# Kernel tuning notes

Hardware: AMD Instinct MI355X
Metric: run time of the kernel (lower is better)

Reference implementation:

```python
import jax, jax.numpy as jnp
import numpy as np

N = 65536          # nodes
E = N * 7          # edges (avg_degree = n_edge_type = 7)
C_IN = 128
C_OUT = 128
N_EDGE_TYPE = 7
N_NODE_TYPE = 5
FEAT = C_IN + N_NODE_TYPE  # 133, channels after one-hot concat


def setup_inputs() -> dict:
    key = jax.random.key(0)
    k1, k2, k3, k4, k5 = jax.random.split(key, 5)
    x = jax.random.normal(k1, (N, C_IN), dtype=jnp.float32)
    edge_idx = jax.random.randint(k2, (2, E), 0, N, dtype=jnp.int64)
    edge_type = jax.random.randint(k3, (E,), 0, N_EDGE_TYPE, dtype=jnp.int64)
    node_type = jax.random.randint(k4, (N,), 0, N_NODE_TYPE, dtype=jnp.int64)
    # uniform init a la module's reset_parameters
    fan_in = 7 * C_IN
    fan_out = 7 * C_OUT
    a = np.sqrt(3.0) * np.sqrt(2.0 / (fan_in + fan_out))
    weights = jax.random.uniform(k5, (N_EDGE_TYPE * FEAT, C_OUT), dtype=jnp.float32,
                                 minval=-a, maxval=a)
    return {"x": x, "edge_idx": edge_idx, "edge_type": edge_type,
            "node_type": node_type, "weights": weights}


def reference(x, edge_idx, edge_type, node_type, weights):
    # one-hot node type concat (n_node_type > 1 branch)
    one_hot = jax.nn.one_hot(node_type, N_NODE_TYPE, dtype=x.dtype)
    xa = jnp.concatenate([x, one_hot], axis=1)          # [N, FEAT]
    row, col = edge_idx[0], edge_idx[1]
    seg = row * N_EDGE_TYPE + edge_type                 # [E]
    gathered = xa[col]                                  # [E, FEAT]
    num_seg = N * N_EDGE_TYPE
    sums = jax.ops.segment_sum(gathered, seg, num_segments=num_seg)
    cnt = jax.ops.segment_sum(jnp.ones((E,), dtype=xa.dtype), seg, num_segments=num_seg)
    col_data = sums / jnp.maximum(cnt, 1.0)[:, None]    # scatter_mean
    # overwrite self-loop slot (last edge type) with node's own features
    self_idx = jnp.arange(N, dtype=jnp.int64) * N_EDGE_TYPE + (N_EDGE_TYPE - 1)
    col_data = col_data.at[self_idx].set(xa)
    out = col_data.reshape(N, N_EDGE_TYPE * FEAT) @ weights  # [N, C_OUT]
    return out
```

## Files before the change

### kernel.cpp

```cpp
#include <hip/hip_runtime.h>
#include <hip/hip_bf16.h>

#define N_NODES 65536
#define N_EDGES (N_NODES * 7)
#define NSEG    (N_NODES * 7)
#define CAP     12
#define ZROW    65536

typedef short short8 __attribute__((ext_vector_type(8)));
typedef float f32x4  __attribute__((ext_vector_type(4)));

__device__ __forceinline__ unsigned short f2bf(float f) {
    return __builtin_bit_cast(unsigned short, (__bf16)f);
}
__device__ __forceinline__ unsigned pack2(float lo, float hi) {
    return (unsigned)f2bf(lo) | ((unsigned)f2bf(hi) << 16);
}
__device__ __forceinline__ float bflo(unsigned d) { return __uint_as_float(d << 16); }
__device__ __forceinline__ float bfhi(unsigned d) { return __uint_as_float(d & 0xffff0000u); }

__global__ __launch_bounds__(256) void k_big(const float* __restrict__ x,
                                             const int* __restrict__ eidx,
                                             const int* __restrict__ etype,
                                             const int* __restrict__ ntype,
                                             const float* __restrict__ W,
                                             unsigned short* __restrict__ xb,
                                             unsigned short* __restrict__ wb,
                                             unsigned* __restrict__ seg32,
                                             unsigned short* __restrict__ scol) {
    int i = blockIdx.x * 256 + threadIdx.x;

    if (i < N_EDGES) {
        int t = etype[i];
        if (t < 6) {
            int r = eidx[i];
            int c = eidx[N_EDGES + i];
            int u = ntype[c];
            unsigned seg = (unsigned)r * 7u + (unsigned)t;
            unsigned inc = 1u | (1u << (7 + 5 * u));
            unsigned old = atomicAdd(&seg32[seg], inc);
            unsigned slot = old & 0x7fu;
            if (slot < CAP) scol[seg * CAP + slot] = (unsigned short)c;
        }
    }

    {
        int row = i >> 4, mm = i & 15;
        const f32x4* p = reinterpret_cast<const f32x4*>(x + (size_t)row * 128 + mm * 8);
        f32x4 v0 = p[0], v1 = p[1];
        uint4 w;
        w.x = pack2(v0[0], v0[1]); w.y = pack2(v0[2], v0[3]);
        w.z = pack2(v1[0], v1[1]); w.w = pack2(v1[2], v1[3]);
        reinterpret_cast<uint4*>(xb)[i] = w;
    }

    if (i < 16) reinterpret_cast<uint4*>(xb + (size_t)ZROW * 128)[i] = (uint4){0u, 0u, 0u, 0u};

    if (i < 143360) {
        int j    = i & 7;
        int lane = (i >> 3) & 63;
        int cb   = (i >> 9) & 7;
        int tkc  = i >> 12;
        int kc   = tkc % 5;
        int t    = tkc / 5;
        int k = kc * 32 + ((lane >> 4) << 3) + j;
        int c = cb * 16 + (lane & 15);
        float v = (k < 133) ? W[(t * 133 + k) * 128 + c] : 0.0f;
        wb[i] = f2bf(v);
    }
}

__global__ __launch_bounds__(512, 4) void k_main(const unsigned short* __restrict__ xb,
                                                 const int* __restrict__ ntype,
                                                 const unsigned* __restrict__ seg32,
                                                 const unsigned short* __restrict__ scol,
                                                 const unsigned short* __restrict__ wb,
                                                 float* __restrict__ out) {
    __shared__ unsigned short sA[3 * 64 * 168];

    const int tid  = threadIdx.x;
    const int lane = tid & 63;
    const int wid  = tid >> 6;
    const int n0   = blockIdx.x * 64;
    const int r    = tid >> 3;
    const int m    = tid & 7;
    const int n    = n0 + r;
    const int wswz = ((r >> 3) & 1) << 5;

    if (tid < 192) {
        uint4 z = {0u, 0u, 0u, 0u};
        *reinterpret_cast<uint4*>(sA + tid * 168 + 136) = z;
        *reinterpret_cast<uint4*>(sA + tid * 168 + 144) = z;
        *reinterpret_cast<uint4*>(sA + tid * 168 + 152) = z;
    }

    unsigned sv[6], c_t[6];
    uint2 q2[6];
    #pragma unroll
    for (int t = 0; t < 6; ++t) {
        sv[t]  = seg32[n * 7 + t];
        c_t[t] = sv[t] & 0x7fu;
        q2[t]  = *reinterpret_cast<const uint2*>(scol + ((size_t)n * 7 + t) * CAP);
    }
    const int ntS = ntype[n];

    auto addrow = [&](float* f, unsigned col) {
        const short8* p = reinterpret_cast<const short8*>(xb + (size_t)col * 128 + m * 16);
        short8 v0 = p[0], v1 = p[1];
        uint4 u0 = *reinterpret_cast<const uint4*>(&v0);
        uint4 u1 = *reinterpret_cast<const uint4*>(&v1);
        f[0] += bflo(u0.x); f[1] += bfhi(u0.x); f[2]  += bflo(u0.y); f[3]  += bfhi(u0.y);
        f[4] += bflo(u0.z); f[5] += bfhi(u0.z); f[6]  += bflo(u0.w); f[7]  += bfhi(u0.w);
        f[8] += bflo(u1.x); f[9] += bfhi(u1.x); f[10] += bflo(u1.y); f[11] += bfhi(u1.y);
        f[12]+= bflo(u1.z); f[13]+= bfhi(u1.z); f[14] += bflo(u1.w); f[15] += bfhi(u1.w);
    };

    auto build_tile = [&](int t, int tile) {
        const unsigned cntv = c_t[t];
        const float inv = (cntv > 1u) ? __builtin_amdgcn_rcpf((float)cntv) : 1.0f;
        unsigned cA = (cntv >= 1u) ? (q2[t].x & 0xffffu) : (unsigned)ZROW;
        unsigned cB = (cntv >= 2u) ? (q2[t].x >> 16)     : (unsigned)ZROW;
        const short8* pA = reinterpret_cast<const short8*>(xb + (size_t)cA * 128 + m * 16);
        const short8* pB = reinterpret_cast<const short8*>(xb + (size_t)cB * 128 + m * 16);
        short8 a0 = pA[0], a1 = pA[1];
        short8 b0 = pB[0], b1 = pB[1];
        uint4 w0, w1;
        if (cntv <= 1u) {
            w0 = *reinterpret_cast<const uint4*>(&a0);
            w1 = *reinterpret_cast<const uint4*>(&a1);
        } else {
            uint4 ua0 = *reinterpret_cast<const uint4*>(&a0);
            uint4 ua1 = *reinterpret_cast<const uint4*>(&a1);
            uint4 ub0 = *reinterpret_cast<const uint4*>(&b0);
            uint4 ub1 = *reinterpret_cast<const uint4*>(&b1);
            float f[16];
            f[0] = bflo(ua0.x)+bflo(ub0.x); f[1] = bfhi(ua0.x)+bfhi(ub0.x);
            f[2] = bflo(ua0.y)+bflo(ub0.y); f[3] = bfhi(ua0.y)+bfhi(ub0.y);
            f[4] = bflo(ua0.z)+bflo(ub0.z); f[5] = bfhi(ua0.z)+bfhi(ub0.z);
            f[6] = bflo(ua0.w)+bflo(ub0.w); f[7] = bfhi(ua0.w)+bfhi(ub0.w);
            f[8] = bflo(ua1.x)+bflo(ub1.x); f[9] = bfhi(ua1.x)+bfhi(ub1.x);
            f[10]= bflo(ua1.y)+bflo(ub1.y); f[11]= bfhi(ua1.y)+bfhi(ub1.y);
            f[12]= bflo(ua1.z)+bflo(ub1.z); f[13]= bfhi(ua1.z)+bfhi(ub1.z);
            f[14]= bflo(ua1.w)+bflo(ub1.w); f[15]= bfhi(ua1.w)+bfhi(ub1.w);
            if (cntv >= 3u) {
                const unsigned ce = (cntv < (unsigned)CAP) ? cntv : (unsigned)CAP;
                addrow(f, q2[t].y & 0xffffu);
                if (ce >= 4u) {
                    addrow(f, q2[t].y >> 16);
                    const size_t segbase = ((size_t)n * 7 + t) * CAP;
                    for (unsigned e = 4; e < ce; ++e)
                        addrow(f, (unsigned)scol[segbase + e]);
                }
            }
            w0.x = pack2(f[0]*inv,  f[1]*inv);  w0.y = pack2(f[2]*inv,  f[3]*inv);
            w0.z = pack2(f[4]*inv,  f[5]*inv);  w0.w = pack2(f[6]*inv,  f[7]*inv);
            w1.x = pack2(f[8]*inv,  f[9]*inv);  w1.y = pack2(f[10]*inv, f[11]*inv);
            w1.z = pack2(f[12]*inv, f[13]*inv); w1.w = pack2(f[14]*inv, f[15]*inv);
        }
        const int base = (tile * 64 + r) * 168;
        const int o = (m * 16) ^ wswz;
        *reinterpret_cast<uint4*>(sA + base + o)     = w0;
        *reinterpret_cast<uint4*>(sA + base + o + 8) = w1;
        if (m == 0) {
            float g0 = (float)((sv[t] >> 7)  & 31u) * inv;
            float g1 = (float)((sv[t] >> 12) & 31u) * inv;
            float g2 = (float)((sv[t] >> 17) & 31u) * inv;
            float g3 = (float)((sv[t] >> 22) & 31u) * inv;
            float g4 = (float)((sv[t] >> 27) & 31u) * inv;
            uint4 wo;
            wo.x = pack2(g0, g1); wo.y = pack2(g2, g3);
            wo.z = pack2(g4, 0.f); wo.w = 0u;
            *reinterpret_cast<uint4*>(sA + base + 128) = wo;
        }
    };

    auto build_self = [&](int tile) {
        const short8* p = reinterpret_cast<const short8*>(xb + (size_t)n * 128 + m * 16);
        short8 s0 = p[0], s1 = p[1];
        const int base = (tile * 64 + r) * 168;
        const int o = (m * 16) ^ wswz;
        *reinterpret_cast<uint4*>(sA + base + o)     = *reinterpret_cast<const uint4*>(&s0);
        *reinterpret_cast<uint4*>(sA + base + o + 8) = *reinterpret_cast<const uint4*>(&s1);
        if (m == 0) {
            uint4 wo;
            wo.x = pack2((float)(ntS == 0), (float)(ntS == 1));
            wo.y = pack2((float)(ntS == 2), (float)(ntS == 3));
            wo.z = pack2((float)(ntS == 4), 0.f);
            wo.w = 0u;
            *reinterpret_cast<uint4*>(sA + base + 128) = wo;
        }
    };

    const int arl  = lane & 15;
    const int g8   = (lane >> 4) << 3;
    const int rswz = ((lane >> 3) & 1) << 5;
    f32x4 acc[4];
    #pragma unroll
    for (int st = 0; st < 4; ++st) acc[st] = (f32x4){0.f, 0.f, 0.f, 0.f};

    auto marathon = [&](int slot, int bt) {
        short8 bv[5];
        #pragma unroll
        for (int kc = 0; kc < 5; ++kc)
            bv[kc] = *reinterpret_cast<const short8*>(
                wb + ((((bt * 5 + kc) * 8 + wid) << 6) + lane) * 8);
        #pragma unroll
        for (int kc = 0; kc < 5; ++kc) {
            const int off = (kc < 4) ? ((kc * 32 + g8) ^ rswz) : (128 + g8);
            #pragma unroll
            for (int st = 0; st < 4; ++st) {
                short8 av = *reinterpret_cast<const short8*>(
                    sA + (slot * 64 + st * 16 + arl) * 168 + off);
                acc[st] = __builtin_amdgcn_mfma_f32_16x16x32_bf16(av, bv[kc], acc[st], 0, 0, 0);
            }
        }
    };

    build_tile(0, 0);
    build_tile(1, 1);
    build_self(2);
    __syncthreads();
    marathon(0, 0); marathon(1, 1); marathon(2, 6);
    __syncthreads();

    build_tile(2, 0);
    build_tile(3, 1);
    __syncthreads();
    marathon(0, 2); marathon(1, 3);
    __syncthreads();

    build_tile(4, 0);
    build_tile(5, 1);
    __syncthreads();
    marathon(0, 4); marathon(1, 5);

    const int ocol = (wid << 4) + (lane & 15);
    const int ro   = ((lane >> 4) << 2);
    #pragma unroll
    for (int st = 0; st < 4; ++st) {
        #pragma unroll
        for (int rr = 0; rr < 4; ++rr) {
            out[(size_t)(n0 + st * 16 + ro + rr) * 128 + ocol] = acc[st][rr];
        }
    }
}


extern "C" void kernel_launch(void* const* d_in, const int* in_sizes, int n_in,
                              void* d_out, int out_size, void* d_ws, size_t ws_size,
                              hipStream_t stream) {
    const float* x     = (const float*)d_in[0];
    const int*   eidx  = (const int*)d_in[1];
    const int*   etype = (const int*)d_in[2];
    const int*   ntype = (const int*)d_in[3];
    const float* W     = (const float*)d_in[4];
    float* out = (float*)d_out;

    unsigned short* xb    = (unsigned short*)d_ws;
    unsigned short* wb    = (unsigned short*)((char*)d_ws + 16777472);
    unsigned*       seg32 = (unsigned*)((char*)d_ws + 17064192);
    unsigned short* scol  = (unsigned short*)((char*)d_ws + 18899200);

    hipMemsetAsync(seg32, 0, NSEG * sizeof(unsigned), stream);
    k_big <<<4096,         256, 0, stream>>>(x, eidx, etype, ntype, W, xb, wb, seg32, scol);
    k_main<<<N_NODES / 64, 512, 0, stream>>>(xb, ntype, seg32, scol, wb, out);
}
```

Before: 83.53 us.

## Split main kernel into producer/consumer waves with double-buffered LDS tiles

Reworks k_main so that four waves gather and average neighbour rows into a double-buffered shared tile while the other four waves run MFMAs on the previous edge-type tile. The block now covers 32 nodes instead of 64, LDS shrinks, and launch bounds rise to 6 blocks per CU. The aim is to overlap the irregular gather latency with matrix compute and raise occupancy. In exchange only half the waves do MFMA, there are more barriers per block, weights are reloaded per 32 rows, and the LDS XOR swizzle was removed, which may add bank conflicts.

```diff
diff --git a/kernel.cpp b/kernel.cpp
--- a/kernel.cpp
+++ b/kernel.cpp
@@ -70,80 +70,73 @@
     }
 }
 
-__global__ __launch_bounds__(512, 4) void k_main(const unsigned short* __restrict__ xb,
+__global__ __launch_bounds__(512, 6) void k_main(const unsigned short* __restrict__ xb,
                                                  const int* __restrict__ ntype,
                                                  const unsigned* __restrict__ seg32,
                                                  const unsigned short* __restrict__ scol,
                                                  const unsigned short* __restrict__ wb,
                                                  float* __restrict__ out) {
-    __shared__ unsigned short sA[3 * 64 * 168];
+    __shared__ unsigned short sA[2][32][168];
 
     const int tid  = threadIdx.x;
     const int lane = tid & 63;
     const int wid  = tid >> 6;
-    const int n0   = blockIdx.x * 64;
-    const int r    = tid >> 3;
-    const int m    = tid & 7;
-    const int n    = n0 + r;
-    const int wswz = ((r >> 3) & 1) << 5;
+    const int n0   = blockIdx.x * 32;
+    const bool consumer = (wid >= 4);
 
     if (tid < 192) {
-        uint4 z = {0u, 0u, 0u, 0u};
-        *reinterpret_cast<uint4*>(sA + tid * 168 + 136) = z;
-        *reinterpret_cast<uint4*>(sA + tid * 168 + 144) = z;
-        *reinterpret_cast<uint4*>(sA + tid * 168 + 152) = z;
-    }
-
-    unsigned sv[6], c_t[6];
-    uint2 q2[6];
-    #pragma unroll
-    for (int t = 0; t < 6; ++t) {
-        sv[t]  = seg32[n * 7 + t];
-        c_t[t] = sv[t] & 0x7fu;
-        q2[t]  = *reinterpret_cast<const uint2*>(scol + ((size_t)n * 7 + t) * CAP);
-    }
-    const int ntS = ntype[n];
+        int j = tid % 3, sr = tid / 3;
+        *reinterpret_cast<uint4*>(&sA[sr >> 5][sr & 31][136 + j * 8]) =
+            (uint4){0u, 0u, 0u, 0u};
+    }
+
+    const int r = (tid >> 3) & 31;
+    const int m = tid & 7;
+    const int n = n0 + r;
+    unsigned sv[6]; uint2 q2[6]; int ntS = 0;
+    if (!consumer) {
+        #pragma unroll
+        for (int t = 0; t < 6; ++t) {
+            sv[t] = seg32[n * 7 + t];
+            q2[t] = *reinterpret_cast<const uint2*>(scol + ((size_t)n * 7 + t) * CAP);
+        }
+        ntS = ntype[n];
+    }
 
     auto addrow = [&](float* f, unsigned col) {
-        const short8* p = reinterpret_cast<const short8*>(xb + (size_t)col * 128 + m * 16);
-        short8 v0 = p[0], v1 = p[1];
-        uint4 u0 = *reinterpret_cast<const uint4*>(&v0);
-        uint4 u1 = *reinterpret_cast<const uint4*>(&v1);
+        const uint4* p = reinterpret_cast<const uint4*>(xb + (size_t)col * 128 + m * 16);
+        uint4 u0 = p[0], u1 = p[1];
         f[0] += bflo(u0.x); f[1] += bfhi(u0.x); f[2]  += bflo(u0.y); f[3]  += bfhi(u0.y);
         f[4] += bflo(u0.z); f[5] += bfhi(u0.z); f[6]  += bflo(u0.w); f[7]  += bfhi(u0.w);
         f[8] += bflo(u1.x); f[9] += bfhi(u1.x); f[10] += bflo(u1.y); f[11] += bfhi(u1.y);
         f[12]+= bflo(u1.z); f[13]+= bfhi(u1.z); f[14] += bflo(u1.w); f[15] += bfhi(u1.w);
     };
 
-    auto build_tile = [&](int t, int tile) {
-        const unsigned cntv = c_t[t];
-        const float inv = (cntv > 1u) ? __builtin_amdgcn_rcpf((float)cntv) : 1.0f;
-        unsigned cA = (cntv >= 1u) ? (q2[t].x & 0xffffu) : (unsigned)ZROW;
-        unsigned cB = (cntv >= 2u) ? (q2[t].x >> 16)     : (unsigned)ZROW;
-        const short8* pA = reinterpret_cast<const short8*>(xb + (size_t)cA * 128 + m * 16);
-        const short8* pB = reinterpret_cast<const short8*>(xb + (size_t)cB * 128 + m * 16);
-        short8 a0 = pA[0], a1 = pA[1];
-        short8 b0 = pB[0], b1 = pB[1];
+    auto build_tile = [&](int t, int slot) {
+        const unsigned svt = sv[t];
+        const unsigned cnt = svt & 0x7fu;
+        const float inv = (cnt > 1u) ? __builtin_amdgcn_rcpf((float)cnt) : 1.0f;
+        unsigned c0 = (cnt >= 1u) ? (q2[t].x & 0xffffu) : (unsigned)ZROW;
+        unsigned c1 = (cnt >= 2u) ? (q2[t].x >> 16)     : (unsigned)ZROW;
+        const uint4* p0 = reinterpret_cast<const uint4*>(xb + (size_t)c0 * 128 + m * 16);
+        const uint4* p1 = reinterpret_cast<const uint4*>(xb + (size_t)c1 * 128 + m * 16);
+        uint4 a0 = p0[0], a1 = p0[1];
+        uint4 b0 = p1[0], b1 = p1[1];
         uint4 w0, w1;
-        if (cntv <= 1u) {
-            w0 = *reinterpret_cast<const uint4*>(&a0);
-            w1 = *reinterpret_cast<const uint4*>(&a1);
+        if (cnt <= 1u) {
+            w0 = a0; w1 = a1;
         } else {
-            uint4 ua0 = *reinterpret_cast<const uint4*>(&a0);
-            uint4 ua1 = *reinterpret_cast<const uint4*>(&a1);
-            uint4 ub0 = *reinterpret_cast<const uint4*>(&b0);
-            uint4 ub1 = *reinterpret_cast<const uint4*>(&b1);
             float f[16];
-            f[0] = bflo(ua0.x)+bflo(ub0.x); f[1] = bfhi(ua0.x)+bfhi(ub0.x);
-            f[2] = bflo(ua0.y)+bflo(ub0.y); f[3] = bfhi(ua0.y)+bfhi(ub0.y);
-            f[4] = bflo(ua0.z)+bflo(ub0.z); f[5] = bfhi(ua0.z)+bfhi(ub0.z);
-            f[6] = bflo(ua0.w)+bflo(ub0.w); f[7] = bfhi(ua0.w)+bfhi(ub0.w);
-            f[8] = bflo(ua1.x)+bflo(ub1.x); f[9] = bfhi(ua1.x)+bfhi(ub1.x);
-            f[10]= bflo(ua1.y)+bflo(ub1.y); f[11]= bfhi(ua1.y)+bfhi(ub1.y);
-            f[12]= bflo(ua1.z)+bflo(ub1.z); f[13]= bfhi(ua1.z)+bfhi(ub1.z);
-            f[14]= bflo(ua1.w)+bflo(ub1.w); f[15]= bfhi(ua1.w)+bfhi(ub1.w);
-            if (cntv >= 3u) {
-                const unsigned ce = (cntv < (unsigned)CAP) ? cntv : (unsigned)CAP;
+            f[0] = bflo(a0.x)+bflo(b0.x); f[1] = bfhi(a0.x)+bfhi(b0.x);
+            f[2] = bflo(a0.y)+bflo(b0.y); f[3] = bfhi(a0.y)+bfhi(b0.y);
+            f[4] = bflo(a0.z)+bflo(b0.z); f[5] = bfhi(a0.z)+bfhi(b0.z);
+            f[6] = bflo(a0.w)+bflo(b0.w); f[7] = bfhi(a0.w)+bfhi(b0.w);
+            f[8] = bflo(a1.x)+bflo(b1.x); f[9] = bfhi(a1.x)+bfhi(b1.x);
+            f[10]= bflo(a1.y)+bflo(b1.y); f[11]= bfhi(a1.y)+bfhi(b1.y);
+            f[12]= bflo(a1.z)+bflo(b1.z); f[13]= bfhi(a1.z)+bfhi(b1.z);
+            f[14]= bflo(a1.w)+bflo(b1.w); f[15]= bfhi(a1.w)+bfhi(b1.w);
+            if (cnt >= 3u) {
+                const unsigned ce = (cnt < (unsigned)CAP) ? cnt : (unsigned)CAP;
                 addrow(f, q2[t].y & 0xffffu);
                 if (ce >= 4u) {
                     addrow(f, q2[t].y >> 16);
@@ -157,90 +150,82 @@
             w1.x = pack2(f[8]*inv,  f[9]*inv);  w1.y = pack2(f[10]*inv, f[11]*inv);
             w1.z = pack2(f[12]*inv, f[13]*inv); w1.w = pack2(f[14]*inv, f[15]*inv);
         }
-        const int base = (tile * 64 + r) * 168;
-        const int o = (m * 16) ^ wswz;
-        *reinterpret_cast<uint4*>(sA + base + o)     = w0;
-        *reinterpret_cast<uint4*>(sA + base + o + 8) = w1;
+        uint4* dst = reinterpret_cast<uint4*>(&sA[slot][r][m * 16]);
+        dst[0] = w0;
+        dst[1] = w1;
         if (m == 0) {
-            float g0 = (float)((sv[t] >> 7)  & 31u) * inv;
-            float g1 = (float)((sv[t] >> 12) & 31u) * inv;
-            float g2 = (float)((sv[t] >> 17) & 31u) * inv;
-            float g3 = (float)((sv[t] >> 22) & 31u) * inv;
-            float g4 = (float)((sv[t] >> 27) & 31u) * inv;
+            float g0 = (float)((svt >> 7)  & 31u) * inv;
+            float g1 = (float)((svt >> 12) & 31u) * inv;
+            float g2 = (float)((svt >> 17) & 31u) * inv;
+            float g3 = (float)((svt >> 22) & 31u) * inv;
+            float g4 = (float)((svt >> 27) & 31u) * inv;
             uint4 wo;
             wo.x = pack2(g0, g1); wo.y = pack2(g2, g3);
             wo.z = pack2(g4, 0.f); wo.w = 0u;
-            *reinterpret_cast<uint4*>(sA + base + 128) = wo;
+            *reinterpret_cast<uint4*>(&sA[slot][r][128]) = wo;
         }
     };
 
-    auto build_self = [&](int tile) {
-        const short8* p = reinterpret_cast<const short8*>(xb + (size_t)n * 128 + m * 16);
-        short8 s0 = p[0], s1 = p[1];
-        const int base = (tile * 64 + r) * 168;
-        const int o = (m * 16) ^ wswz;
-        *reinterpret_cast<uint4*>(sA + base + o)     = *reinterpret_cast<const uint4*>(&s0);
-        *reinterpret_cast<uint4*>(sA + base + o + 8) = *reinterpret_cast<const uint4*>(&s1);
+    auto build_self = [&](int slot) {
+        const uint4* p = reinterpret_cast<const uint4*>(xb + (size_t)n * 128 + m * 16);
+        uint4 s0 = p[0], s1 = p[1];
+        uint4* dst = reinterpret_cast<uint4*>(&sA[slot][r][m * 16]);
+        dst[0] = s0;
+        dst[1] = s1;
         if (m == 0) {
             uint4 wo;
             wo.x = pack2((float)(ntS == 0), (float)(ntS == 1));
             wo.y = pack2((float)(ntS == 2), (float)(ntS == 3));
             wo.z = pack2((float)(ntS == 4), 0.f);
             wo.w = 0u;
-            *reinterpret_cast<uint4*>(sA + base + 128) = wo;
+            *reinterpret_cast<uint4*>(&sA[slot][r][128]) = wo;
         }
     };
 
-    const int arl  = lane & 15;
-    const int g8   = (lane >> 4) << 3;
-    const int rswz = ((lane >> 3) & 1) << 5;
-    f32x4 acc[4];
+    const int p   = wid - 4;
+    const int arl = lane & 15;
+    const int g8  = (lane >> 4) << 3;
+    f32x4 acc00 = {0.f,0.f,0.f,0.f}, acc01 = {0.f,0.f,0.f,0.f};
+    f32x4 acc10 = {0.f,0.f,0.f,0.f}, acc11 = {0.f,0.f,0.f,0.f};
+
+    if (!consumer) build_tile(0, 0);
+    __syncthreads();
+
     #pragma unroll
-    for (int st = 0; st < 4; ++st) acc[st] = (f32x4){0.f, 0.f, 0.f, 0.f};
-
-    auto marathon = [&](int slot, int bt) {
-        short8 bv[5];
-        #pragma unroll
-        for (int kc = 0; kc < 5; ++kc)
-            bv[kc] = *reinterpret_cast<const short8*>(
-                wb + ((((bt * 5 + kc) * 8 + wid) << 6) + lane) * 8);
-        #pragma unroll
-        for (int kc = 0; kc < 5; ++kc) {
-            const int off = (kc < 4) ? ((kc * 32 + g8) ^ rswz) : (128 + g8);
+    for (int t = 0; t < 7; ++t) {
+        if (consumer) {
+            const int slot = t & 1;
             #pragma unroll
-            for (int st = 0; st < 4; ++st) {
-                short8 av = *reinterpret_cast<const short8*>(
-                    sA + (slot * 64 + st * 16 + arl) * 168 + off);
-                acc[st] = __builtin_amdgcn_mfma_f32_16x16x32_bf16(av, bv[kc], acc[st], 0, 0, 0);
+            for (int kc = 0; kc < 5; ++kc) {
+                short8 b0 = *reinterpret_cast<const short8*>(
+                    wb + ((((t * 5 + kc) * 8 + 2 * p) << 6) + lane) * 8);
+                short8 b1 = *reinterpret_cast<const short8*>(
+                    wb + ((((t * 5 + kc) * 8 + 2 * p + 1) << 6) + lane) * 8);
+                short8 a0 = *reinterpret_cast<const short8*>(
+                    &sA[slot][arl][kc * 32 + g8]);
+                short8 a1 = *reinterpret_cast<const short8*>(
+                    &sA[slot][16 + arl][kc * 32 + g8]);
+                acc00 = __builtin_amdgcn_mfma_f32_16x16x32_bf16(a0, b0, acc00, 0, 0, 0);
+                acc01 = __builtin_amdgcn_mfma_f32_16x16x32_bf16(a0, b1, acc01, 0, 0, 0);
+                acc10 = __builtin_amdgcn_mfma_f32_16x16x32_bf16(a1, b0, acc10, 0, 0, 0);
+                acc11 = __builtin_amdgcn_mfma_f32_16x16x32_bf16(a1, b1, acc11, 0, 0, 0);
             }
-        }
-    };
-
-    build_tile(0, 0);
-    build_tile(1, 1);
-    build_self(2);
-    __syncthreads();
-    marathon(0, 0); marathon(1, 1); marathon(2, 6);
-    __syncthreads();
-
-    build_tile(2, 0);
-    build_tile(3, 1);
-    __syncthreads();
-    marathon(0, 2); marathon(1, 3);
-    __syncthreads();
-
-    build_tile(4, 0);
-    build_tile(5, 1);
-    __syncthreads();
-    marathon(0, 4); marathon(1, 5);
-
-    const int ocol = (wid << 4) + (lane & 15);
-    const int ro   = ((lane >> 4) << 2);
-    #pragma unroll
-    for (int st = 0; st < 4; ++st) {
+        } else {
+            if (t < 5)       build_tile(t + 1, (t + 1) & 1);
+            else if (t == 5) build_self(0);
+        }
+        if (t < 6) __syncthreads();
+    }
+
+    if (consumer) {
+        const int ro = (lane >> 4) << 2;
+        const int oc = (2 * p) * 16 + (lane & 15);
         #pragma unroll
         for (int rr = 0; rr < 4; ++rr) {
-            out[(size_t)(n0 + st * 16 + ro + rr) * 128 + ocol] = acc[st][rr];
+            out[(size_t)(n0 + ro + rr) * 128 + oc]           = acc00[rr];
+            out[(size_t)(n0 + ro + rr) * 128 + oc + 16]      = acc01[rr];
+            out[(size_t)(n0 + 16 + ro + rr) * 128 + oc]      = acc10[rr];
+            out[(size_t)(n0 + 16 + ro + rr) * 128 + oc + 16] = acc11[rr];
         }
     }
 }
@@ -263,5 +248,5 @@
 
     hipMemsetAsync(seg32, 0, NSEG * sizeof(unsigned), stream);
     k_big <<<4096,         256, 0, stream>>>(x, eidx, etype, ntype, W, xb, wb, seg32, scol);
-    k_main<<<N_NODES / 64, 512, 0, stream>>>(xb, ntype, seg32, scol, wb, out);
-}
+    k_main<<<N_NODES / 32, 512, 0, stream>>>(xb, ntype, seg32, scol, wb, out);
+}
```

New measurement: 84.07 us. Within noise of the previous version (+0.6%).
